# Optimization experiments

Hardware: AMD Instinct MI355X
Metric: run time of the kernel (lower is better)

## Reference

```python
import jax, jax.numpy as jnp
import numpy as np

VOC_SHAPE = (100, 100, 100)   # m_k factors of voc_size = 1_000_000
EMB_SHAPE = (4, 4, 8)         # n_k factors of emb_size = 128
RANK = 16
PAD_IDX = 0
VOC = int(np.prod(VOC_SHAPE))
EMB = int(np.prod(EMB_SHAPE))


def setup_inputs() -> dict:
    key = jax.random.key(0)
    k0, k1, k2, kx = jax.random.split(key, 4)
    # TT-matrix cores [r_k, m_k, n_k, r_{k+1}], boundary ranks = 1.
    # Per-core std chosen so the reconstructed table has stddev near
    # target_stddev = sqrt(2/voc_size) (the 'nn' init intent); exact init
    # distribution is irrelevant to the math being tested.
    d = 3
    target_std = np.sqrt(2.0 / VOC)
    core_std = float((target_std / RANK ** ((d - 1) / 2.0)) ** (1.0 / d))
    core0 = jax.random.normal(k0, (1, VOC_SHAPE[0], EMB_SHAPE[0], RANK), jnp.float32) * core_std
    core1 = jax.random.normal(k1, (RANK, VOC_SHAPE[1], EMB_SHAPE[1], RANK), jnp.float32) * core_std
    core2 = jax.random.normal(k2, (RANK, VOC_SHAPE[2], EMB_SHAPE[2], 1), jnp.float32) * core_std
    x = jax.random.randint(kx, (64, 512), 0, VOC, dtype=jnp.int64)
    return {"x": x, "core0": core0, "core1": core1, "core2": core2}


def _tt_full(core0, core1, core2):
    # Sequential TT-matrix contraction, as in sample_full():
    # res accumulates shape (m1*n1*...*mk*nk, r_{k+1})
    res = core0.reshape(-1, core0.shape[-1])                      # (m1*n1, r1)
    res = res @ core1.reshape(core1.shape[0], -1)                 # (m1*n1, m2*n2*r2)
    res = res.reshape(-1, core2.shape[0]) @ core2.reshape(core2.shape[0], -1)
    # (m1, n1, m2, n2, m3, n3) -> (m1, m2, m3, n1, n2, n3) -> (VOC, EMB)
    m1, m2, m3 = VOC_SHAPE
    n1, n2, n3 = EMB_SHAPE
    full = res.reshape(m1, n1, m2, n2, m3, n3)
    full = full.transpose(0, 2, 4, 1, 3, 5).reshape(VOC, EMB)
    return full


def reference(x, core0, core1, core2):
    xshape = x.shape
    x_flat = x.reshape(-1)
    full = _tt_full(core0, core1, core2)          # [VOC, EMB] materialized table
    rows = full[x_flat]                           # gather [B*S, EMB]
    rows = jnp.where(x_flat[:, None] != PAD_IDX, rows, jnp.zeros_like(rows))
    return rows.reshape(*xshape, EMB)
```

## Files before the change

### kernel.cpp

```cpp
#include <hip/hip_runtime.h>


#define AB_STRIDE 68
#define LDS_PER_WAVE (4 * AB_STRIDE)

__global__ __launch_bounds__(256) void tt_embed_kernel(
    const int* __restrict__ x,
    const float* __restrict__ c0,
    const float* __restrict__ c1,
    const float* __restrict__ c2,
    float* __restrict__ out,
    int nTok)
{
    __shared__ __align__(16) float lds[4 * LDS_PER_WAVE];
    const int wave = threadIdx.x >> 6;
    const int lane = threadIdx.x & 63;
    const int t = blockIdx.x * 4 + wave;
    const bool active = (t < nTok);

    float* ABs = lds + wave * LDS_PER_WAVE;

    int idx = 0;
    if (active) idx = x[t];
    idx = __builtin_amdgcn_readfirstlane(idx);
    const int i1 = idx / 10000;
    const int rem = idx - i1 * 10000;
    const int i2 = rem / 100;
    const int i3 = rem - i2 * 100;

    const float* cA = c0 + i1 * 64;
    const float* Bb = c1 + i2 * 64 + lane;

    float ab0 = 0.f, ab1 = 0.f, ab2 = 0.f, ab3 = 0.f;
    #pragma unroll
    for (int r1 = 0; r1 < 16; ++r1) {
        const float b = Bb[r1 * 6400];
        ab0 += cA[r1]      * b;
        ab1 += cA[16 + r1] * b;
        ab2 += cA[32 + r1] * b;
        ab3 += cA[48 + r1] * b;
    }

    ABs[0 * AB_STRIDE + lane] = ab0;
    ABs[1 * AB_STRIDE + lane] = ab1;
    ABs[2 * AB_STRIDE + lane] = ab2;
    ABs[3 * AB_STRIDE + lane] = ab3;

    const int j3 = (lane & 3) * 2;
    const float* Cb = c2 + i3 * 8 + j3;
    float cvx[16], cvy[16];
    #pragma unroll
    for (int r2 = 0; r2 < 16; ++r2) {
        const float2 cv = *(const float2*)(Cb + r2 * 800);
        cvx[r2] = cv.x; cvy[r2] = cv.y;
    }

    asm volatile("s_waitcnt lgkmcnt(0)" ::: "memory");

    const int j1w = lane >> 4;
    const int j2w = (lane >> 2) & 3;
    const float4* abp = (const float4*)(ABs + j1w * AB_STRIDE + j2w * 16);
    float4 q0 = abp[0], q1 = abp[1], q2 = abp[2], q3 = abp[3];
    float ab[16] = { q0.x,q0.y,q0.z,q0.w, q1.x,q1.y,q1.z,q1.w,
                     q2.x,q2.y,q2.z,q2.w, q3.x,q3.y,q3.z,q3.w };

    float o0 = 0.f, o1 = 0.f;
    #pragma unroll
    for (int r2 = 0; r2 < 16; ++r2) {
        o0 += ab[r2] * cvx[r2];
        o1 += ab[r2] * cvy[r2];
    }

    if (idx == 0) { o0 = 0.f; o1 = 0.f; }

    if (active) {
        const int e0 = lane * 2;
        *(float2*)(out + (long)t * 128 + e0) = make_float2(o0, o1);
    }
}

extern "C" void kernel_launch(void* const* d_in, const int* in_sizes, int n_in,
                              void* d_out, int out_size, void* d_ws, size_t ws_size,
                              hipStream_t stream) {
    const int*   x  = (const int*)d_in[0];
    const float* c0 = (const float*)d_in[1];
    const float* c1 = (const float*)d_in[2];
    const float* c2 = (const float*)d_in[3];
    float* out = (float*)d_out;

    const int nTok = out_size / 128;
    const int blocks = (nTok + 3) / 4;
    tt_embed_kernel<<<dim3(blocks), dim3(256), 0, stream>>>(x, c0, c1, c2, out, nTok);
}
```

Before: 85.10 us.

## Replace LDS staging with butterfly shuffle reduction over rank dimension

Removes the LDS round-trip for the intermediate core0·core1 product. Each lane instead loads one rank slice of core2 with two vector loads, forms 32 partial products, and reduces across lanes with a recursive-halving xor-shuffle butterfly. The output element mapping per lane is rearranged to match. This cuts c2 global loads per lane and the LDS traffic, but adds about 30 cross-lane shuffles and extra register pressure.

```diff
diff --git a/kernel.cpp b/kernel.cpp
--- a/kernel.cpp
+++ b/kernel.cpp
@@ -1,8 +1,5 @@
 #include <hip/hip_runtime.h>
 
-
-#define AB_STRIDE 68
-#define LDS_PER_WAVE (4 * AB_STRIDE)
 
 __global__ __launch_bounds__(256) void tt_embed_kernel(
     const int* __restrict__ x,
@@ -12,13 +9,10 @@
     float* __restrict__ out,
     int nTok)
 {
-    __shared__ __align__(16) float lds[4 * LDS_PER_WAVE];
     const int wave = threadIdx.x >> 6;
     const int lane = threadIdx.x & 63;
     const int t = blockIdx.x * 4 + wave;
     const bool active = (t < nTok);
-
-    float* ABs = lds + wave * LDS_PER_WAVE;
 
     int idx = 0;
     if (active) idx = x[t];
@@ -27,6 +21,11 @@
     const int rem = idx - i1 * 10000;
     const int i2 = rem / 100;
     const int i3 = rem - i2 * 100;
+
+    const int r2 = lane & 15;
+
+    const float4* Cp = (const float4*)(c2 + (r2 * 100 + i3) * 8);
+    float4 cl = Cp[0], ch = Cp[1];
 
     const float* cA = c0 + i1 * 64;
     const float* Bb = c1 + i2 * 64 + lane;
@@ -41,41 +40,58 @@
         ab3 += cA[48 + r1] * b;
     }
 
-    ABs[0 * AB_STRIDE + lane] = ab0;
-    ABs[1 * AB_STRIDE + lane] = ab1;
-    ABs[2 * AB_STRIDE + lane] = ab2;
-    ABs[3 * AB_STRIDE + lane] = ab3;
+    const float ab[4] = { ab0, ab1, ab2, ab3 };
+    const float cr[8] = { cl.x, cl.y, cl.z, cl.w, ch.x, ch.y, ch.z, ch.w };
+    float p[32];
+    #pragma unroll
+    for (int a = 0; a < 4; ++a)
+        #pragma unroll
+        for (int j = 0; j < 8; ++j)
+            p[a * 8 + j] = ab[a] * cr[j];
 
-    const int j3 = (lane & 3) * 2;
-    const float* Cb = c2 + i3 * 8 + j3;
-    float cvx[16], cvy[16];
+    const bool s0 = (lane >> 3) & 1;
+    float q[16];
     #pragma unroll
-    for (int r2 = 0; r2 < 16; ++r2) {
-        const float2 cv = *(const float2*)(Cb + r2 * 800);
-        cvx[r2] = cv.x; cvy[r2] = cv.y;
+    for (int k = 0; k < 16; ++k) {
+        const float send = s0 ? p[k] : p[k + 16];
+        const float keep = s0 ? p[k + 16] : p[k];
+        q[k] = keep + __shfl_xor(send, 8);
     }
-
-    asm volatile("s_waitcnt lgkmcnt(0)" ::: "memory");
-
-    const int j1w = lane >> 4;
-    const int j2w = (lane >> 2) & 3;
-    const float4* abp = (const float4*)(ABs + j1w * AB_STRIDE + j2w * 16);
-    float4 q0 = abp[0], q1 = abp[1], q2 = abp[2], q3 = abp[3];
-    float ab[16] = { q0.x,q0.y,q0.z,q0.w, q1.x,q1.y,q1.z,q1.w,
-                     q2.x,q2.y,q2.z,q2.w, q3.x,q3.y,q3.z,q3.w };
-
-    float o0 = 0.f, o1 = 0.f;
+    const bool s1 = (lane >> 2) & 1;
+    float r_[8];
     #pragma unroll
-    for (int r2 = 0; r2 < 16; ++r2) {
-        o0 += ab[r2] * cvx[r2];
-        o1 += ab[r2] * cvy[r2];
+    for (int k = 0; k < 8; ++k) {
+        const float send = s1 ? q[k] : q[k + 8];
+        const float keep = s1 ? q[k + 8] : q[k];
+        r_[k] = keep + __shfl_xor(send, 4);
+    }
+    const bool s2 = (lane >> 1) & 1;
+    float s_[4];
+    #pragma unroll
+    for (int k = 0; k < 4; ++k) {
+        const float send = s2 ? r_[k] : r_[k + 4];
+        const float keep = s2 ? r_[k + 4] : r_[k];
+        s_[k] = keep + __shfl_xor(send, 2);
+    }
+    const bool s3 = lane & 1;
+    float o0, o1;
+    {
+        const float send0 = s3 ? s_[0] : s_[2];
+        const float keep0 = s3 ? s_[2] : s_[0];
+        o0 = keep0 + __shfl_xor(send0, 1);
+        const float send1 = s3 ? s_[1] : s_[3];
+        const float keep1 = s3 ? s_[3] : s_[1];
+        o1 = keep1 + __shfl_xor(send1, 1);
     }
 
     if (idx == 0) { o0 = 0.f; o1 = 0.f; }
 
     if (active) {
-        const int e0 = lane * 2;
-        *(float2*)(out + (long)t * 128 + e0) = make_float2(o0, o1);
+        const int j1 = (int)s0 * 2 + (int)s1;
+        const int j3 = (int)s2 * 4 + (int)s3 * 2;
+        const int j2 = lane >> 4;
+        const int e  = j1 * 32 + j2 * 8 + j3;
+        *(float2*)(out + (long)t * 128 + e) = make_float2(o0, o1);
     }
 }
 
```

Result: faster. 77.67 us (-8.7%).
